# Kernel tuning notes

Measured on AMD Instinct MI355X. Metric: run time of the kernel, lower is better.

Reference implementation:

```python
import jax, jax.numpy as jnp
import numpy as np

TAU = 2.0          # LIF membrane time constant (spikingjelly default)
ALPHA = 2.0        # ATan surrogate width
EPS = 1e-5         # BatchNorm eps
NUM_HEADS = 8
SCALE = 0.125

@jax.custom_vjp
def spike(x):
    return (x >= 0.0).astype(x.dtype)

def _spike_fwd(x):
    return (x >= 0.0).astype(x.dtype), x

def _spike_bwd(x, g):
    # ATan surrogate gradient (spikingjelly default)
    return (g * (ALPHA / 2.0) / (1.0 + (jnp.pi / 2.0 * ALPHA * x) ** 2),)

spike.defvjp(_spike_fwd, _spike_bwd)

def lif(x, v_th):
    # Multi-step LIF over leading time axis T; hard reset to 0, v_reset=0.
    def step(v, xt):
        h = v + (xt - v) / TAU
        s = spike(h - v_th)
        return h * (1.0 - s), s
    _, s = jax.lax.scan(step, jnp.zeros_like(x[0]), x)
    return s

def bn(x, g, b, m, v):
    # BatchNorm1d in eval mode over channel (last) dim
    return (x - m) * jax.lax.rsqrt(v + EPS) * g + b

def setup_inputs() -> dict:
    key = jax.random.key(0)
    ks = jax.random.split(key, 16)
    T, B, N, C = 4, 16, 512, 512
    s = 1.0 / np.sqrt(C)
    inp = {"x": jax.random.normal(ks[0], (T, B, N, C), jnp.float32)}
    for i, p in enumerate("qkvp"):
        inp[f"w{p}"] = jax.random.normal(ks[1 + i], (C, C), jnp.float32) * s
        inp[f"b{p}"] = jnp.zeros((C,), jnp.float32)
        inp[f"{p}_gamma"] = jnp.ones((C,), jnp.float32)
        inp[f"{p}_beta"] = jnp.zeros((C,), jnp.float32)
        inp[f"{p}_mean"] = jax.random.normal(ks[5 + i], (C,), jnp.float32) * 0.1
        inp[f"{p}_var"] = jax.random.uniform(ks[9 + i], (C,), jnp.float32, minval=0.5, maxval=1.5)
    return inp

def reference(x, wq, bq, q_gamma, q_beta, q_mean, q_var,
              wk, bk, k_gamma, k_beta, k_mean, k_var,
              wv, bv, v_gamma, v_beta, v_mean, v_var,
              wp, bp, p_gamma, p_beta, p_mean, p_var):
    T, B, N, C = x.shape
    H = NUM_HEADS
    D = C // H

    def branch(w, b, g, be, m, va):
        y = bn(x @ w.T + b, g, be, m, va)          # Linear -> BN1d (eval)
        y = lif(y, 1.0)                             # spiking activation
        return y.reshape(T, B, N, H, D).transpose(0, 1, 3, 2, 4)  # [T,B,H,N,D]

    q = branch(wq, bq, q_gamma, q_beta, q_mean, q_var)
    k = branch(wk, bk, k_gamma, k_beta, k_mean, k_var)
    v = branch(wv, bv, v_gamma, v_beta, v_mean, v_var)

    attn = jnp.einsum('tbhnd,tbhmd->tbhnm', q, k) * SCALE  # [T,B,H,N,N]
    o = jnp.einsum('tbhnm,tbhmd->tbhnd', attn, v)          # [T,B,H,N,D]
    o = o.transpose(0, 1, 3, 2, 4).reshape(T, B, N, C)
    o = lif(o, 0.5)                                        # attn_lif, v_th=0.5
    o = bn(o @ wp.T + bp, p_gamma, p_beta, p_mean, p_var)
    return lif(o, 1.0)
```

## Files before the change

### kernel.cpp

```cpp
#include <hip/hip_runtime.h>
#include <hip/hip_bf16.h>
#include <hip/hip_fp16.h>
#include <cstddef>
#include <cstdint>

#define T_ 4
#define B_ 16
#define N_ 512
#define C_ 512
#define H_ 8
#define D_ 64
#define BN_T (B_*N_)

typedef unsigned short u16;
typedef __attribute__((ext_vector_type(8))) short bf16x8;
typedef __attribute__((ext_vector_type(8))) _Float16 f16x8;
typedef __attribute__((ext_vector_type(8))) unsigned short u16x8;
typedef __attribute__((ext_vector_type(4))) float f32x4;

__device__ __forceinline__ u16 f2bf_exact(float f) {
    union { float f; unsigned u; } x; x.f = f; return (u16)(x.u >> 16);
}
__device__ __forceinline__ void split2(float f, u16& h1, u16& h2) {
    const __half a = __float2half(f);
    const float r = (f - __half2float(a)) * 2048.0f;
    const __half b = __float2half(r);
    h1 = __half_as_ushort(a); h2 = __half_as_ushort(b);
}
__device__ __forceinline__ int swz(int rr, int q) {
    return (rr << 6) + (((q ^ ((rr >> 1) & 3)) & 3) << 4);
}
__device__ __forceinline__ int SW(int row, int col) {
    return (row << 6) + (col ^ ((row & 7) << 3));
}
__device__ __forceinline__ void gload16(const void* g, void* l) {
    __builtin_amdgcn_global_load_lds(
        (const __attribute__((address_space(1))) unsigned int*)g,
        (__attribute__((address_space(3))) unsigned int*)l, 16, 0, 0);
}

#define PHASE3T(p, STAGE, WAIT) do {                                          \
    const int cc_ = 64 * wc + 16 * (p);                                       \
    const int rrB_ = (cc_ & 127) + l15;                                       \
    const char* LB_ = L + (2 + (cc_ >> 7)) * 8192;                            \
    const f16x8 b1_ = *reinterpret_cast<const f16x8*>(LB_ + swz(rrB_, g));    \
    const f16x8 b2_ = *reinterpret_cast<const f16x8*>(LB_ + 16384 + swz(rrB_, g)); \
    STAGE;                                                                    \
    WAIT;                                                                     \
    __builtin_amdgcn_sched_barrier(0);                                        \
    __builtin_amdgcn_s_barrier();                                             \
    asm volatile("s_waitcnt lgkmcnt(0)" ::: "memory");                        \
    __builtin_amdgcn_sched_barrier(0);                                        \
    __builtin_amdgcn_s_setprio(1);                                            \
    _Pragma("unroll")                                                         \
    for (int rt_ = 0; rt_ < 4; ++rt_) {                                       \
        accA[rt_][p] = __builtin_amdgcn_mfma_f32_16x16x32_f16(a1[rt_], b1_, accA[rt_][p], 0, 0, 0); \
        accB[rt_][p] = __builtin_amdgcn_mfma_f32_16x16x32_f16(a2[rt_], b1_, accB[rt_][p], 0, 0, 0); \
        accB[rt_][p] = __builtin_amdgcn_mfma_f32_16x16x32_f16(a1[rt_], b2_, accB[rt_][p], 0, 0, 0); \
    }                                                                         \
    __builtin_amdgcn_s_setprio(0);                                            \
    __builtin_amdgcn_s_barrier();                                             \
} while (0)

#define PHASE2T(p, STAGE, WAIT) do {                                          \
    const int cc_ = 64 * wc + 16 * (p);                                       \
    const int rrB_ = (cc_ & 127) + l15;                                       \
    const char* LB_ = L + (1 + (cc_ >> 7)) * 8192;                            \
    const f16x8 b1_ = *reinterpret_cast<const f16x8*>(LB_ + swz(rrB_, g));    \
    const f16x8 b2_ = *reinterpret_cast<const f16x8*>(LB_ + 16384 + swz(rrB_, g)); \
    STAGE;                                                                    \
    WAIT;                                                                     \
    __builtin_amdgcn_sched_barrier(0);                                        \
    __builtin_amdgcn_s_barrier();                                             \
    asm volatile("s_waitcnt lgkmcnt(0)" ::: "memory");                        \
    __builtin_amdgcn_sched_barrier(0);                                        \
    __builtin_amdgcn_s_setprio(1);                                            \
    _Pragma("unroll")                                                         \
    for (int rt_ = 0; rt_ < 4; ++rt_) {                                       \
        accA[rt_][p] = __builtin_amdgcn_mfma_f32_16x16x32_f16(a1[rt_], b1_, accA[rt_][p], 0, 0, 0); \
        accB[rt_][p] = __builtin_amdgcn_mfma_f32_16x16x32_f16(a1[rt_], b2_, accB[rt_][p], 0, 0, 0); \
    }                                                                         \
    __builtin_amdgcn_s_setprio(0);                                            \
    __builtin_amdgcn_s_barrier();                                             \
} while (0)

__global__ __launch_bounds__(256) void k_split_x(
    const float* __restrict__ x, u16* __restrict__ x1t, u16* __restrict__ x2t)
{
    const int tile = blockIdx.x;
    const int mt = tile >> 4, kb = tile & 15;
    const int tid = threadIdx.x;
    const int rr = tid >> 1, kh = tid & 1;
    const int t = rr & 3, bn = mt * 32 + (rr >> 2);
    const float* src = x + ((size_t)t * BN_T + bn) * C_ + kb * 32 + kh * 16;
    float f[16];
    *reinterpret_cast<float4*>(f + 0)  = *reinterpret_cast<const float4*>(src + 0);
    *reinterpret_cast<float4*>(f + 4)  = *reinterpret_cast<const float4*>(src + 4);
    *reinterpret_cast<float4*>(f + 8)  = *reinterpret_cast<const float4*>(src + 8);
    *reinterpret_cast<float4*>(f + 12) = *reinterpret_cast<const float4*>(src + 12);
    char* d1 = (char*)(x1t + ((size_t)tile << 12));
    char* d2 = (char*)(x2t + ((size_t)tile << 12));
    #pragma unroll
    for (int j = 0; j < 2; ++j) {
        u16x8 p1, p2;
        #pragma unroll
        for (int e = 0; e < 8; ++e) { u16 h1, h2; split2(f[8*j+e], h1, h2); p1[e] = h1; p2[e] = h2; }
        const int q = 2 * kh + j;
        *reinterpret_cast<u16x8*>(d1 + swz(rr, q)) = p1;
        *reinterpret_cast<u16x8*>(d2 + swz(rr, q)) = p2;
    }
}

__global__ __launch_bounds__(256) void k_split_w(
    const float* __restrict__ w, u16* __restrict__ w1t, u16* __restrict__ w2t)
{
    const int tile = blockIdx.x;
    const int nt = tile >> 4, kb = tile & 15;
    const int tid = threadIdx.x;
    const int rr = tid >> 1, kh = tid & 1;
    const int c = nt * 128 + rr;
    const float* src = w + (size_t)c * C_ + kb * 32 + kh * 16;
    float f[16];
    *reinterpret_cast<float4*>(f + 0)  = *reinterpret_cast<const float4*>(src + 0);
    *reinterpret_cast<float4*>(f + 4)  = *reinterpret_cast<const float4*>(src + 4);
    *reinterpret_cast<float4*>(f + 8)  = *reinterpret_cast<const float4*>(src + 8);
    *reinterpret_cast<float4*>(f + 12) = *reinterpret_cast<const float4*>(src + 12);
    char* d1 = (char*)(w1t + ((size_t)tile << 12));
    char* d2 = (char*)(w2t + ((size_t)tile << 12));
    #pragma unroll
    for (int j = 0; j < 2; ++j) {
        u16x8 p1, p2;
        #pragma unroll
        for (int e = 0; e < 8; ++e) { u16 h1, h2; split2(f[8*j+e], h1, h2); p1[e] = h1; p2[e] = h2; }
        const int q = 2 * kh + j;
        *reinterpret_cast<u16x8*>(d1 + swz(rr, q)) = p1;
        *reinterpret_cast<u16x8*>(d2 + swz(rr, q)) = p2;
    }
}

__global__ __launch_bounds__(512, 2) void k_linear_qkv(
    const u16* __restrict__ a1t, const u16* __restrict__ a2t,
    const u16* __restrict__ wt_base,
    const float* __restrict__ bi0, const float* __restrict__ ga0, const float* __restrict__ be0,
    const float* __restrict__ mu0, const float* __restrict__ va0,
    const float* __restrict__ bi1, const float* __restrict__ ga1, const float* __restrict__ be1,
    const float* __restrict__ mu1, const float* __restrict__ va1,
    const float* __restrict__ bi2, const float* __restrict__ ga2, const float* __restrict__ be2,
    const float* __restrict__ mu2, const float* __restrict__ va2,
    u16* __restrict__ oq, u16* __restrict__ ok, u16* __restrict__ ov)
{
    __shared__ u16 lds[3][6][4096];

    const int dd  = blockIdx.x;
    const int lid = (dd & 7) * 192 + (dd >> 3);
    const int mt  = lid / 6;
    const int rem = lid - mt * 6;
    const int li  = rem >> 1;
    const int nt  = rem & 1;
    const int bn0 = mt * 32;
    const int c0  = nt * 256;

    const float* bias  = li == 0 ? bi0 : li == 1 ? bi1 : bi2;
    const float* gamma = li == 0 ? ga0 : li == 1 ? ga1 : ga2;
    const float* beta  = li == 0 ? be0 : li == 1 ? be1 : be2;
    const float* mean  = li == 0 ? mu0 : li == 1 ? mu1 : mu2;
    const float* var   = li == 0 ? va0 : li == 1 ? va1 : va2;
    u16* outp = li == 0 ? oq : li == 1 ? ok : ov;

    const size_t WSZ = (size_t)C_ * C_;
    const u16* w1t = wt_base + (size_t)(2 * li) * WSZ;
    const u16* w2t = wt_base + (size_t)(2 * li + 1) * WSZ;

    const int tid = threadIdx.x;
    const int wv  = tid >> 6, lane = tid & 63;
    const int l15 = lane & 15, g = (lane >> 4) & 3;
    const int wr  = wv >> 2, wc = wv & 3;
    const int so  = tid * 16;

    f32x4 accA[4][4], accB[4][4];
    #pragma unroll
    for (int rt = 0; rt < 4; ++rt)
        #pragma unroll
        for (int ct = 0; ct < 4; ++ct) { accA[rt][ct] = {0,0,0,0}; accB[rt][ct] = {0,0,0,0}; }

    const size_t abase  = (size_t)mt * 16;
    const size_t bbase0 = (size_t)(nt * 2 + 0) * 16;
    const size_t bbase1 = (size_t)(nt * 2 + 1) * 16;
    char* const L0 = (char*)&lds[0][0][0];

    auto sA = [&](int kb) { char* Ls = L0 + (kb % 3) * 49152;
        gload16((const char*)(a1t + ((abase  + kb) << 12)) + so, Ls + 0 * 8192 + so);
        gload16((const char*)(a2t + ((abase  + kb) << 12)) + so, Ls + 1 * 8192 + so); };
    auto sB1 = [&](int kb) { char* Ls = L0 + (kb % 3) * 49152;
        gload16((const char*)(w1t + ((bbase0 + kb) << 12)) + so, Ls + 2 * 8192 + so);
        gload16((const char*)(w1t + ((bbase1 + kb) << 12)) + so, Ls + 3 * 8192 + so); };
    auto sB2 = [&](int kb) { char* Ls = L0 + (kb % 3) * 49152;
        gload16((const char*)(w2t + ((bbase0 + kb) << 12)) + so, Ls + 4 * 8192 + so);
        gload16((const char*)(w2t + ((bbase1 + kb) << 12)) + so, Ls + 5 * 8192 + so); };

    sA(0); sB1(0); sB2(0);
    sA(1); sB1(1); sB2(1);
    __builtin_amdgcn_sched_barrier(0);
    asm volatile("s_waitcnt vmcnt(6)" ::: "memory");
    __builtin_amdgcn_s_barrier();
    __builtin_amdgcn_sched_barrier(0);

    #pragma unroll 1
    for (int k = 0; k < 16; ++k) {
        const char* L = L0 + (k % 3) * 49152;
        f16x8 a1[4], a2[4];
        #pragma unroll
        for (int rt = 0; rt < 4; ++rt) {
            const int rr = 64 * wr + 16 * rt + l15;
            a1[rt] = *reinterpret_cast<const f16x8*>(L + swz(rr, g));
            a2[rt] = *reinterpret_cast<const f16x8*>(L + 8192 + swz(rr, g));
        }
        const bool st = (k <= 13);
        PHASE3T(0, if (st) sA(k + 2), );
        PHASE3T(1, if (st) sB1(k + 2), );
        PHASE3T(2, if (st) sB2(k + 2), );
        if (k < 14) { PHASE3T(3, , asm volatile("s_waitcnt vmcnt(6)" ::: "memory")); }
        else        { PHASE3T(3, , asm volatile("s_waitcnt vmcnt(0)" ::: "memory")); }
    }

    #pragma unroll
    for (int ct = 0; ct < 4; ++ct) {
        const int c = c0 + 64 * wc + 16 * ct + l15;
        const float rs = 1.0f / sqrtf(var[c] + 1e-5f);
        const float ga = gamma[c], be = beta[c], mu = mean[c], bi = bias[c];
        #pragma unroll
        for (int rt = 0; rt < 4; ++rt) {
            const int bn = bn0 + 16 * wr + 4 * rt + g;
            float vm = 0.f;
            #pragma unroll
            for (int r = 0; r < 4; ++r) {
                const float y = accA[rt][ct][r] + accB[rt][ct][r] * (1.0f / 2048.0f) + bi;
                const float ybn = (y - mu) * rs * ga + be;
                const float h = vm + (ybn - vm) * 0.5f;
                const bool sp = (h >= 1.0f);
                vm = sp ? 0.f : h;
                const int b = bn >> 9, n = bn & 511;
                const int hh = c >> 6, d2 = c & 63;
                outp[((((size_t)r * B_ + b) * H_ + hh) * N_ + n) * D_ + d2] = sp ? 0x3F80 : 0;
            }
        }
    }
}

__global__ __launch_bounds__(512, 2) void k_linear_out(
    const u16* __restrict__ a1t,
    const u16* __restrict__ w1t, const u16* __restrict__ w2t,
    const float* __restrict__ bias, const float* __restrict__ gamma,
    const float* __restrict__ beta, const float* __restrict__ mean,
    const float* __restrict__ var, float* __restrict__ outp)
{
    __shared__ u16 lds[3][5][4096];

    const int dd  = blockIdx.x;
    const int lid = (dd & 7) * 64 + (dd >> 3);
    const int mt  = lid >> 1;
    const int nt  = lid & 1;
    const int bn0 = mt * 32;
    const int c0  = nt * 256;

    const int tid = threadIdx.x;
    const int wv  = tid >> 6, lane = tid & 63;
    const int l15 = lane & 15, g = (lane >> 4) & 3;
    const int wr  = wv >> 2, wc = wv & 3;
    const int so  = tid * 16;

    f32x4 accA[4][4], accB[4][4];
    #pragma unroll
    for (int rt = 0; rt < 4; ++rt)
        #pragma unroll
        for (int ct = 0; ct < 4; ++ct) { accA[rt][ct] = {0,0,0,0}; accB[rt][ct] = {0,0,0,0}; }

    const size_t abase  = (size_t)mt * 16;
    const size_t bbase0 = (size_t)(nt * 2 + 0) * 16;
    const size_t bbase1 = (size_t)(nt * 2 + 1) * 16;
    char* const L0 = (char*)&lds[0][0][0];

    auto s0 = [&](int kb) { char* Ls = L0 + (kb % 3) * 40960;
        gload16((const char*)(a1t + ((abase  + kb) << 12)) + so, Ls + 0 * 8192 + so);
        gload16((const char*)(w1t + ((bbase0 + kb) << 12)) + so, Ls + 1 * 8192 + so); };
    auto s1 = [&](int kb) { char* Ls = L0 + (kb % 3) * 40960;
        gload16((const char*)(w1t + ((bbase1 + kb) << 12)) + so, Ls + 2 * 8192 + so);
        gload16((const char*)(w2t + ((bbase0 + kb) << 12)) + so, Ls + 3 * 8192 + so); };
    auto s2 = [&](int kb) { char* Ls = L0 + (kb % 3) * 40960;
        gload16((const char*)(w2t + ((bbase1 + kb) << 12)) + so, Ls + 4 * 8192 + so); };

    s0(0); s1(0); s2(0);
    s0(1); s1(1); s2(1);
    __builtin_amdgcn_sched_barrier(0);
    asm volatile("s_waitcnt vmcnt(5)" ::: "memory");
    __builtin_amdgcn_s_barrier();
    __builtin_amdgcn_sched_barrier(0);

    #pragma unroll 1
    for (int k = 0; k < 16; ++k) {
        const char* L = L0 + (k % 3) * 40960;
        f16x8 a1[4];
        #pragma unroll
        for (int rt = 0; rt < 4; ++rt) {
            const int rr = 64 * wr + 16 * rt + l15;
            a1[rt] = *reinterpret_cast<const f16x8*>(L + swz(rr, g));
        }
        const bool st = (k <= 13);
        PHASE2T(0, if (st) s0(k + 2), );
        PHASE2T(1, if (st) s1(k + 2), );
        PHASE2T(2, if (st) s2(k + 2), );
        if (k < 14) { PHASE2T(3, , asm volatile("s_waitcnt vmcnt(5)" ::: "memory")); }
        else        { PHASE2T(3, , asm volatile("s_waitcnt vmcnt(0)" ::: "memory")); }
    }

    #pragma unroll
    for (int ct = 0; ct < 4; ++ct) {
        const int c = c0 + 64 * wc + 16 * ct + l15;
        const float rs = 1.0f / sqrtf(var[c] + 1e-5f);
        const float ga = gamma[c], be = beta[c], mu = mean[c], bi = bias[c];
        #pragma unroll
        for (int rt = 0; rt < 4; ++rt) {
            const int bn = bn0 + 16 * wr + 4 * rt + g;
            float vm = 0.f;
            #pragma unroll
            for (int r = 0; r < 4; ++r) {
                const float y = accA[rt][ct][r] + accB[rt][ct][r] * (1.0f / 2048.0f) + bi;
                const float ybn = (y - mu) * rs * ga + be;
                const float h = vm + (ybn - vm) * 0.5f;
                const bool sp = (h >= 1.0f);
                vm = sp ? 0.f : h;
                outp[((size_t)r * BN_T + bn) * C_ + c] = sp ? 1.0f : 0.0f;
            }
        }
    }
}

__global__ __launch_bounds__(512, 2) void k_attn_mfma(
    const u16* __restrict__ qg, const u16* __restrict__ kg,
    const u16* __restrict__ vg, u16* __restrict__ s2t)
{
    __shared__ u16 kf[8][4096];
    __shared__ u16 vf[8][4096];
    __shared__ u16 ssb[8][1024];

    const int id  = blockIdx.x;
    const int lid = (id & 7) * 64 + (id >> 3);
    const int bh  = lid >> 2;
    const int qt  = lid & 3;
    const int b   = bh >> 3, hh = bh & 7;

    const int tid  = threadIdx.x;
    const int w    = tid >> 6, lane = tid & 63;
    const int l15  = lane & 15, g = lane >> 4;

    const int vkv = (tid & 15) * 4;
    const int vd  = ((tid >> 4) & 15) * 4;

    bf16x8 qa[2];
    f32x4 vmem[4], oacc[4];
    #pragma unroll
    for (int d0 = 0; d0 < 4; ++d0) { vmem[d0] = {0,0,0,0}; oacc[d0] = {0,0,0,0}; }

    #pragma unroll 1
    for (int t = 0; t < T_; ++t) {
        const size_t base = ((size_t)t * (B_ * H_) + bh) * (size_t)(N_ * D_);
        if (t > 0) __syncthreads();

        {
            const size_t qrow = base + (size_t)(qt * 128 + 16 * w + l15) * D_;
            qa[0] = *reinterpret_cast<const bf16x8*>(qg + qrow + 8 * g);
            qa[1] = *reinterpret_cast<const bf16x8*>(qg + qrow + 32 + 8 * g);
        }
        {
            const u16* kb = kg + base;
            #pragma unroll
            for (int i = 0; i < 8; ++i) {
                const int r64 = tid >> 3;
                const int col = (tid & 7) * 8;
                const u16x8 v = *reinterpret_cast<const u16x8*>(kb + ((size_t)(tid + 512 * i)) * 8);
                *reinterpret_cast<u16x8*>(&kf[i][SW(r64, col)]) = v;
            }
        }
        {
            const u16* vb = vg + base;
            #pragma unroll
            for (int i = 0; i < 4; ++i) {
                const int jt = 2 * i + (tid >> 8);
                const int m0 = jt * 64;
                ushort4 r0 = *reinterpret_cast<const ushort4*>(vb + (size_t)(m0 + vkv + 0) * D_ + vd);
                ushort4 r1 = *reinterpret_cast<const ushort4*>(vb + (size_t)(m0 + vkv + 1) * D_ + vd);
                ushort4 r2 = *reinterpret_cast<const ushort4*>(vb + (size_t)(m0 + vkv + 2) * D_ + vd);
                ushort4 r3 = *reinterpret_cast<const ushort4*>(vb + (size_t)(m0 + vkv + 3) * D_ + vd);
                ushort4 wv4;
                wv4.x = r0.x; wv4.y = r1.x; wv4.z = r2.x; wv4.w = r3.x;
                *reinterpret_cast<ushort4*>(&vf[jt][SW(vd + 0, vkv)]) = wv4;
                wv4.x = r0.y; wv4.y = r1.y; wv4.z = r2.y; wv4.w = r3.y;
                *reinterpret_cast<ushort4*>(&vf[jt][SW(vd + 1, vkv)]) = wv4;
                wv4.x = r0.z; wv4.y = r1.z; wv4.z = r2.z; wv4.w = r3.z;
                *reinterpret_cast<ushort4*>(&vf[jt][SW(vd + 2, vkv)]) = wv4;
                wv4.x = r0.w; wv4.y = r1.w; wv4.z = r2.w; wv4.w = r3.w;
                *reinterpret_cast<ushort4*>(&vf[jt][SW(vd + 3, vkv)]) = wv4;
            }
        }
        __syncthreads();

        u16* sb = &ssb[w][0];
        #pragma unroll
        for (int jt = 0; jt < 8; ++jt) {
            __builtin_amdgcn_s_setprio(1);
            #pragma unroll
            for (int kvt = 0; kvt < 2; ++kvt) {
                f32x4 acc = {0.f, 0.f, 0.f, 0.f};
                #pragma unroll
                for (int c = 0; c < 2; ++c) {
                    const bf16x8 kb = *reinterpret_cast<const bf16x8*>(
                        &kf[jt][SW(16 * kvt + l15, 32 * c + 8 * g)]);
                    acc = __builtin_amdgcn_mfma_f32_16x16x32_bf16(qa[c], kb, acc, 0, 0, 0);
                }
                #pragma unroll
                for (int r = 0; r < 4; ++r)
                    sb[SW(4 * g + r, 16 * kvt + l15)] = f2bf_exact(acc[r]);
            }
            {
                const bf16x8 sa = *reinterpret_cast<const bf16x8*>(&sb[SW(l15, 8 * g)]);
                #pragma unroll
                for (int d0 = 0; d0 < 4; ++d0) {
                    const bf16x8 vb2 = *reinterpret_cast<const bf16x8*>(
                        &vf[jt][SW(16 * d0 + l15, 8 * g)]);
                    oacc[d0] = __builtin_amdgcn_mfma_f32_16x16x32_bf16(sa, vb2, oacc[d0], 0, 0, 0);
                }
            }
            #pragma unroll
            for (int kvt = 2; kvt < 4; ++kvt) {
                f32x4 acc = {0.f, 0.f, 0.f, 0.f};
                #pragma unroll
                for (int c = 0; c < 2; ++c) {
                    const bf16x8 kb = *reinterpret_cast<const bf16x8*>(
                        &kf[jt][SW(16 * kvt + l15, 32 * c + 8 * g)]);
                    acc = __builtin_amdgcn_mfma_f32_16x16x32_bf16(qa[c], kb, acc, 0, 0, 0);
                }
                #pragma unroll
                for (int r = 0; r < 4; ++r)
                    sb[SW(4 * g + r, 16 * kvt + l15)] = f2bf_exact(acc[r]);
            }
            {
                const bf16x8 sa = *reinterpret_cast<const bf16x8*>(&sb[SW(l15, 32 + 8 * g)]);
                #pragma unroll
                for (int d0 = 0; d0 < 4; ++d0) {
                    const bf16x8 vb2 = *reinterpret_cast<const bf16x8*>(
                        &vf[jt][SW(16 * d0 + l15, 32 + 8 * g)]);
                    oacc[d0] = __builtin_amdgcn_mfma_f32_16x16x32_bf16(sa, vb2, oacc[d0], 0, 0, 0);
                }
            }
            __builtin_amdgcn_s_setprio(0);
        }

        #pragma unroll
        for (int d0 = 0; d0 < 4; ++d0) {
            const int c = hh * 64 + d0 * 16 + l15;
            const int kb2 = c >> 5, kq = (c >> 3) & 3, e = c & 7;
            #pragma unroll
            for (int r = 0; r < 4; ++r) {
                const float o = oacc[d0][r] * 0.125f;
                const float h = vmem[d0][r] + (o - vmem[d0][r]) * 0.5f;
                const bool sp = (h >= 0.5f);
                vmem[d0][r] = sp ? 0.f : h;
                const int n = qt * 128 + 16 * w + 4 * g + r;
                const int bn = b * 512 + n;
                const int mt2 = bn >> 5;
                const int rr2 = (bn & 31) * 4 + t;
                const size_t off = (((size_t)mt2 * 16 + kb2) << 13) + (rr2 << 6)
                                 + (((kq ^ ((rr2 >> 1) & 3)) & 3) << 4) + (e << 1);
                *(u16*)((char*)s2t + off) = sp ? 0x3C00 : 0;
            }
            oacc[d0] = {0.f, 0.f, 0.f, 0.f};
        }
    }
}

extern "C" void kernel_launch(void* const* d_in, const int* in_sizes, int n_in,
                              void* d_out, int out_size, void* d_ws, size_t ws_size,
                              hipStream_t stream)
{
    const float* x = (const float*)d_in[0];
    const float* W[4]  = {(const float*)d_in[1],  (const float*)d_in[7],  (const float*)d_in[13], (const float*)d_in[19]};
    const float* Bi[4] = {(const float*)d_in[2],  (const float*)d_in[8],  (const float*)d_in[14], (const float*)d_in[20]};
    const float* Ga[4] = {(const float*)d_in[3],  (const float*)d_in[9],  (const float*)d_in[15], (const float*)d_in[21]};
    const float* Be[4] = {(const float*)d_in[4],  (const float*)d_in[10], (const float*)d_in[16], (const float*)d_in[22]};
    const float* Mu[4] = {(const float*)d_in[5],  (const float*)d_in[11], (const float*)d_in[17], (const float*)d_in[23]};
    const float* Va[4] = {(const float*)d_in[6],  (const float*)d_in[12], (const float*)d_in[18], (const float*)d_in[24]};

    const size_t SPK = (size_t)T_ * B_ * N_ * C_;
    const size_t WSZ = (size_t)C_ * C_;
    u16* qb  = (u16*)d_ws;
    u16* kbf = qb + SPK;
    u16* vbf = kbf + SPK;
    u16* x1t = vbf + SPK;
    u16* x2t = x1t + SPK;
    u16* wt  = x2t + SPK;
    u16* s2t = x1t;

    dim3 blk(256);
    k_split_x<<<4096, blk, 0, stream>>>(x, x1t, x2t);
    for (int i = 0; i < 4; ++i)
        k_split_w<<<64, blk, 0, stream>>>(W[i], wt + (2*i) * WSZ, wt + (2*i+1) * WSZ);

    k_linear_qkv<<<1536, dim3(512), 0, stream>>>(x1t, x2t, wt,
        Bi[0], Ga[0], Be[0], Mu[0], Va[0],
        Bi[1], Ga[1], Be[1], Mu[1], Va[1],
        Bi[2], Ga[2], Be[2], Mu[2], Va[2],
        qb, kbf, vbf);
    k_attn_mfma<<<512, dim3(512), 0, stream>>>(qb, kbf, vbf, s2t);
    k_linear_out<<<512, dim3(512), 0, stream>>>(s2t, wt + 6*WSZ, wt + 7*WSZ,
        Bi[3], Ga[3], Be[3], Mu[3], Va[3], (float*)d_out);
}
```

Baseline: 322.5 us.

## Shrink QKV GEMM tiles to 256 threads with simple double-buffered pipeline

```diff
diff --git a/kernel.cpp b/kernel.cpp
--- a/kernel.cpp
+++ b/kernel.cpp
@@ -38,29 +38,6 @@
         (const __attribute__((address_space(1))) unsigned int*)g,
         (__attribute__((address_space(3))) unsigned int*)l, 16, 0, 0);
 }
-
-#define PHASE3T(p, STAGE, WAIT) do {                                          \
-    const int cc_ = 64 * wc + 16 * (p);                                       \
-    const int rrB_ = (cc_ & 127) + l15;                                       \
-    const char* LB_ = L + (2 + (cc_ >> 7)) * 8192;                            \
-    const f16x8 b1_ = *reinterpret_cast<const f16x8*>(LB_ + swz(rrB_, g));    \
-    const f16x8 b2_ = *reinterpret_cast<const f16x8*>(LB_ + 16384 + swz(rrB_, g)); \
-    STAGE;                                                                    \
-    WAIT;                                                                     \
-    __builtin_amdgcn_sched_barrier(0);                                        \
-    __builtin_amdgcn_s_barrier();                                             \
-    asm volatile("s_waitcnt lgkmcnt(0)" ::: "memory");                        \
-    __builtin_amdgcn_sched_barrier(0);                                        \
-    __builtin_amdgcn_s_setprio(1);                                            \
-    _Pragma("unroll")                                                         \
-    for (int rt_ = 0; rt_ < 4; ++rt_) {                                       \
-        accA[rt_][p] = __builtin_amdgcn_mfma_f32_16x16x32_f16(a1[rt_], b1_, accA[rt_][p], 0, 0, 0); \
-        accB[rt_][p] = __builtin_amdgcn_mfma_f32_16x16x32_f16(a2[rt_], b1_, accB[rt_][p], 0, 0, 0); \
-        accB[rt_][p] = __builtin_amdgcn_mfma_f32_16x16x32_f16(a1[rt_], b2_, accB[rt_][p], 0, 0, 0); \
-    }                                                                         \
-    __builtin_amdgcn_s_setprio(0);                                            \
-    __builtin_amdgcn_s_barrier();                                             \
-} while (0)
 
 #define PHASE2T(p, STAGE, WAIT) do {                                          \
     const int cc_ = 64 * wc + 16 * (p);                                       \
@@ -138,7 +115,7 @@
     }
 }
 
-__global__ __launch_bounds__(512, 2) void k_linear_qkv(
+__global__ __launch_bounds__(256, 2) void k_linear_qkv(
     const u16* __restrict__ a1t, const u16* __restrict__ a2t,
     const u16* __restrict__ wt_base,
     const float* __restrict__ bi0, const float* __restrict__ ga0, const float* __restrict__ be0,
@@ -149,16 +126,16 @@
     const float* __restrict__ mu2, const float* __restrict__ va2,
     u16* __restrict__ oq, u16* __restrict__ ok, u16* __restrict__ ov)
 {
-    __shared__ u16 lds[3][6][4096];
+    __shared__ u16 lds[2][4][4096];
 
     const int dd  = blockIdx.x;
-    const int lid = (dd & 7) * 192 + (dd >> 3);
-    const int mt  = lid / 6;
-    const int rem = lid - mt * 6;
-    const int li  = rem >> 1;
-    const int nt  = rem & 1;
+    const int lid = (dd & 7) * 384 + (dd >> 3);
+    const int mt  = lid / 12;
+    const int ntg = lid - mt * 12;
+    const int li  = ntg >> 2;
+    const int nt  = ntg & 3;
     const int bn0 = mt * 32;
-    const int c0  = nt * 256;
+    const int c0  = nt * 128;
 
     const float* bias  = li == 0 ? bi0 : li == 1 ? bi1 : bi2;
     const float* gamma = li == 0 ? ga0 : li == 1 ? ga1 : ga2;
@@ -174,8 +151,9 @@
     const int tid = threadIdx.x;
     const int wv  = tid >> 6, lane = tid & 63;
     const int l15 = lane & 15, g = (lane >> 4) & 3;
-    const int wr  = wv >> 2, wc = wv & 3;
-    const int so  = tid * 16;
+    const int wr  = wv >> 1, wc = wv & 1;
+    const int go  = wv * 2048 + lane * 16;
+    const int lo  = wv * 2048;
 
     f32x4 accA[4][4], accB[4][4];
     #pragma unroll
@@ -183,31 +161,32 @@
         #pragma unroll
         for (int ct = 0; ct < 4; ++ct) { accA[rt][ct] = {0,0,0,0}; accB[rt][ct] = {0,0,0,0}; }
 
-    const size_t abase  = (size_t)mt * 16;
-    const size_t bbase0 = (size_t)(nt * 2 + 0) * 16;
-    const size_t bbase1 = (size_t)(nt * 2 + 1) * 16;
-    char* const L0 = (char*)&lds[0][0][0];
-
-    auto sA = [&](int kb) { char* Ls = L0 + (kb % 3) * 49152;
-        gload16((const char*)(a1t + ((abase  + kb) << 12)) + so, Ls + 0 * 8192 + so);
-        gload16((const char*)(a2t + ((abase  + kb) << 12)) + so, Ls + 1 * 8192 + so); };
-    auto sB1 = [&](int kb) { char* Ls = L0 + (kb % 3) * 49152;
-        gload16((const char*)(w1t + ((bbase0 + kb) << 12)) + so, Ls + 2 * 8192 + so);
-        gload16((const char*)(w1t + ((bbase1 + kb) << 12)) + so, Ls + 3 * 8192 + so); };
-    auto sB2 = [&](int kb) { char* Ls = L0 + (kb % 3) * 49152;
-        gload16((const char*)(w2t + ((bbase0 + kb) << 12)) + so, Ls + 4 * 8192 + so);
-        gload16((const char*)(w2t + ((bbase1 + kb) << 12)) + so, Ls + 5 * 8192 + so); };
-
-    sA(0); sB1(0); sB2(0);
-    sA(1); sB1(1); sB2(1);
-    __builtin_amdgcn_sched_barrier(0);
-    asm volatile("s_waitcnt vmcnt(6)" ::: "memory");
-    __builtin_amdgcn_s_barrier();
-    __builtin_amdgcn_sched_barrier(0);
+    const size_t abase = (size_t)mt * 16, bbase = (size_t)nt * 16;
+
+    auto stage = [&](int buf, int kb) {
+        char* L = (char*)&lds[buf][0][0];
+        const char* ga1p = (const char*)(a1t + ((abase + kb) << 12)) + go;
+        const char* ga2p = (const char*)(a2t + ((abase + kb) << 12)) + go;
+        const char* gb1 = (const char*)(w1t + ((bbase + kb) << 12)) + go;
+        const char* gb2 = (const char*)(w2t + ((bbase + kb) << 12)) + go;
+        gload16(ga1p,        L + lo);
+        gload16(ga1p + 1024, L + lo + 1024);
+        gload16(ga2p,        L + 8192 + lo);
+        gload16(ga2p + 1024, L + 8192 + lo + 1024);
+        gload16(gb1,        L + 16384 + lo);
+        gload16(gb1 + 1024, L + 16384 + lo + 1024);
+        gload16(gb2,        L + 24576 + lo);
+        gload16(gb2 + 1024, L + 24576 + lo + 1024);
+    };
+
+    stage(0, 0);
+    __syncthreads();
 
     #pragma unroll 1
-    for (int k = 0; k < 16; ++k) {
-        const char* L = L0 + (k % 3) * 49152;
+    for (int kb = 0; kb < 16; ++kb) {
+        const int buf = kb & 1;
+        if (kb < 15) stage(buf ^ 1, kb + 1);
+        const char* L = (const char*)&lds[buf][0][0];
         f16x8 a1[4], a2[4];
         #pragma unroll
         for (int rt = 0; rt < 4; ++rt) {
@@ -215,12 +194,19 @@
             a1[rt] = *reinterpret_cast<const f16x8*>(L + swz(rr, g));
             a2[rt] = *reinterpret_cast<const f16x8*>(L + 8192 + swz(rr, g));
         }
-        const bool st = (k <= 13);
-        PHASE3T(0, if (st) sA(k + 2), );
-        PHASE3T(1, if (st) sB1(k + 2), );
-        PHASE3T(2, if (st) sB2(k + 2), );
-        if (k < 14) { PHASE3T(3, , asm volatile("s_waitcnt vmcnt(6)" ::: "memory")); }
-        else        { PHASE3T(3, , asm volatile("s_waitcnt vmcnt(0)" ::: "memory")); }
+        #pragma unroll
+        for (int ct = 0; ct < 4; ++ct) {
+            const int rr2 = 64 * wc + 16 * ct + l15;
+            const f16x8 b1 = *reinterpret_cast<const f16x8*>(L + 16384 + swz(rr2, g));
+            const f16x8 b2 = *reinterpret_cast<const f16x8*>(L + 24576 + swz(rr2, g));
+            #pragma unroll
+            for (int rt = 0; rt < 4; ++rt) {
+                accA[rt][ct] = __builtin_amdgcn_mfma_f32_16x16x32_f16(a1[rt], b1, accA[rt][ct], 0, 0, 0);
+                accB[rt][ct] = __builtin_amdgcn_mfma_f32_16x16x32_f16(a2[rt], b1, accB[rt][ct], 0, 0, 0);
+                accB[rt][ct] = __builtin_amdgcn_mfma_f32_16x16x32_f16(a1[rt], b2, accB[rt][ct], 0, 0, 0);
+            }
+        }
+        __syncthreads();
     }
 
     #pragma unroll
@@ -505,7 +491,7 @@
     for (int i = 0; i < 4; ++i)
         k_split_w<<<64, blk, 0, stream>>>(W[i], wt + (2*i) * WSZ, wt + (2*i+1) * WSZ);
 
-    k_linear_qkv<<<1536, dim3(512), 0, stream>>>(x1t, x2t, wt,
+    k_linear_qkv<<<3072, blk, 0, stream>>>(x1t, x2t, wt,
         Bi[0], Ga[0], Be[0], Mu[0], Va[0],
         Bi[1], Ga[1], Be[1], Mu[1], Va[1],
         Bi[2], Ga[2], Be[2], Mu[2], Va[2],
```

Result: faster. 305.3 us (-5.3%).
